# Kernel tuning notes

Hardware: AMD Instinct MI355X
Metric: run time of the kernel (lower is better)

## Reference

```python
import jax, jax.numpy as jnp
import numpy as np

D_MODEL = 768
N_HEADS = 12
D_K = D_MODEL // N_HEADS
NEG = -1e9


def setup_inputs() -> dict:
    key = jax.random.key(0)
    ks = jax.random.split(key, 10)
    B, S = 2, 2048
    x = jax.random.normal(ks[0], (B, S, D_MODEL), dtype=jnp.float32)
    # causal mask, broadcastable over batch and heads
    mask = jnp.tril(jnp.ones((S, S), dtype=jnp.int32))[None, None]
    scale = 1.0 / np.sqrt(D_MODEL)
    def lin(k):
        return jax.random.normal(k, (D_MODEL, D_MODEL), dtype=jnp.float32) * scale
    return {
        "x": x, "mask": mask,
        "wq": lin(ks[1]), "bq": jnp.zeros((D_MODEL,), jnp.float32),
        "wk": lin(ks[2]), "bk": jnp.zeros((D_MODEL,), jnp.float32),
        "wv": lin(ks[3]), "bv": jnp.zeros((D_MODEL,), jnp.float32),
        "wo": lin(ks[4]), "bo": jnp.zeros((D_MODEL,), jnp.float32),
    }


def reference(x, mask, wq, bq, wk, bk, wv, bv, wo, bo):
    B, S, _ = x.shape
    def split_heads(t):  # [B,S,D] -> [B,H,S,dk]
        return t.reshape(B, S, N_HEADS, D_K).transpose(0, 2, 1, 3)
    q = split_heads(x @ wq + bq)
    k = split_heads(x @ wk + bk)
    v = split_heads(x @ wv + bv)
    scores = jnp.einsum("bhqd,bhkd->bhqk", q, k) / jnp.sqrt(jnp.float32(D_K))
    scores = jnp.where(mask == 0, NEG, scores)
    attn = jax.nn.softmax(scores, axis=-1)
    # dropout is identity in eval mode
    ctx = jnp.einsum("bhqk,bhkd->bhqd", attn, v)
    ctx = ctx.transpose(0, 2, 1, 3).reshape(B, S, D_MODEL)
    return ctx @ wo + bo
```

## Files before the change

kernel.cpp:

```cpp
#include <hip/hip_runtime.h>
#include <hip/hip_bf16.h>
#include <stdint.h>

#define DM   768
#define NH   12
#define DKH  64
#define BB   2
#define SS   2048
#define MT   (BB*SS)
#define NQKV (3*DM)

typedef __attribute__((ext_vector_type(8))) short short8;
typedef __attribute__((ext_vector_type(4))) float f32x4;

__device__ __forceinline__ unsigned short f2bf(float f) {
    union { float f; unsigned u; } v; v.f = f;
    unsigned r = v.u + 0x7fffu + ((v.u >> 16) & 1u);
    return (unsigned short)(r >> 16);
}

__device__ __forceinline__ void gload_lds16(const unsigned short* g, unsigned short* l) {
    __builtin_amdgcn_global_load_lds((const __attribute__((address_space(1))) void*)g,
                                     (__attribute__((address_space(3))) void*)l, 16, 0, 0);
}

__launch_bounds__(256)
__global__ void k_conv(const float* __restrict__ x, unsigned short* __restrict__ xb,
                       const float* __restrict__ wq, const float* __restrict__ wk,
                       const float* __restrict__ wv, const float* __restrict__ wo,
                       unsigned short* __restrict__ wT) {
    __shared__ float tile[32][33];
    const int t = threadIdx.x;
    if (blockIdx.x < 3072) {
        int i = blockIdx.x * 256 + t;
        const float4 v = ((const float4*)x)[i];
        ushort4 o;
        o.x = f2bf(v.x); o.y = f2bf(v.y); o.z = f2bf(v.z); o.w = f2bf(v.w);
        ((ushort4*)xb)[i] = o;
    } else {
        const int cid = blockIdx.x - 3072;
        const int sel = cid / 576;
        const int rem = cid - sel * 576;
        const int kb = rem / 24, nb = rem - (rem / 24) * 24;
        const float* w = (sel == 0) ? wq : (sel == 1) ? wk : (sel == 2) ? wv : wo;
        const int k0 = kb * 32, n0 = nb * 32;
        const int tx = t & 31, ty = t >> 5;
        #pragma unroll
        for (int j = 0; j < 4; j++)
            tile[ty + 8*j][tx] = w[(size_t)(k0 + ty + 8*j) * DM + n0 + tx];
        __syncthreads();
        #pragma unroll
        for (int j = 0; j < 4; j++)
            wT[(size_t)(sel*DM + n0 + ty + 8*j) * DM + k0 + tx] = f2bf(tile[tx][ty + 8*j]);
    }
}

__launch_bounds__(256, 4)
__global__ void k_gemm_qkv(const unsigned short* __restrict__ xb,
                           const unsigned short* __restrict__ wT,
                           const float* __restrict__ bq, const float* __restrict__ bk,
                           const float* __restrict__ bv,
                           unsigned short* __restrict__ Qb,
                           unsigned short* __restrict__ Kb,
                           unsigned short* __restrict__ Vt) {
    __shared__ __align__(16) unsigned short As[128*64];
    __shared__ __align__(16) unsigned short Bs[64*64];
    const int t = threadIdx.x;
    const int m0 = blockIdx.x * 128;
    const int n0 = blockIdx.y * 64;
    const int wid = t >> 6, lane = t & 63, q4 = lane >> 4, l16 = lane & 15;
    const int wm = (wid >> 1) * 64, wn = (wid & 1) * 32;

    const int srow = lane >> 3;
    const int scol = ((lane & 7) ^ srow) * 8;
    const unsigned short* Ag = xb + (size_t)(m0 + wid*8 + srow) * DM + scol;
    const unsigned short* Bg = wT + (size_t)(n0 + wid*8 + srow) * DM + scol;
    unsigned short* ldsA = &As[(wid*8)*64];
    unsigned short* ldsB = &Bs[(wid*8)*64];
    const int swz = (l16 & 7) * 8;

    f32x4 acc[4][2];
    for (int i = 0; i < 4; i++) for (int j = 0; j < 2; j++)
        acc[i][j] = (f32x4){0.f, 0.f, 0.f, 0.f};

    for (int kt = 0; kt < DM; kt += 64) {
        #pragma unroll
        for (int j = 0; j < 4; j++)
            gload_lds16(Ag + (size_t)(j*32) * DM + kt, ldsA + j*32*64);
        #pragma unroll
        for (int j = 0; j < 2; j++)
            gload_lds16(Bg + (size_t)(j*32) * DM + kt, ldsB + j*32*64);
        __syncthreads();
        #pragma unroll
        for (int kc = 0; kc < 2; kc++) {
            short8 af[4], bf[2];
            #pragma unroll
            for (int i = 0; i < 4; i++)
                af[i] = *(const short8*)&As[(wm + i*16 + l16)*64 + ((kc*32 + q4*8) ^ swz)];
            #pragma unroll
            for (int i = 0; i < 2; i++)
                bf[i] = *(const short8*)&Bs[(wn + i*16 + l16)*64 + ((kc*32 + q4*8) ^ swz)];
            #pragma unroll
            for (int mi = 0; mi < 4; mi++)
                #pragma unroll
                for (int ni = 0; ni < 2; ni++)
                    acc[mi][ni] = __builtin_amdgcn_mfma_f32_16x16x32_bf16(af[mi], bf[ni], acc[mi][ni], 0, 0, 0);
        }
        __syncthreads();
    }

    const int sel = n0 / DM;
    if (sel < 2) {
        const float* bias = (sel == 0) ? bq : bk;
        for (int ni = 0; ni < 2; ni++) {
            const int col = n0 + wn + ni*16 + l16;
            const int c = col - sel * DM;
            const float bsv = bias[c];
            const int h = c >> 6, d = c & 63;
            for (int mi = 0; mi < 4; mi++) {
                for (int r = 0; r < 4; r++) {
                    const int row = m0 + wm + mi*16 + q4*4 + r;
                    const int b = row >> 11, s = row & 2047;
                    const int bh = b * NH + h;
                    float v = acc[mi][ni][r] + bsv;
                    if (sel == 0) Qb[(bh*SS + s)*DKH + d] = f2bf(v * 0.125f);
                    else          Kb[(bh*SS + s)*DKH + d] = f2bf(v);
                }
            }
        }
    } else {
        const int h  = (n0 - 2*DM) >> 6;
        const int bb = m0 >> 11, sbase = m0 & 2047;
        const int bh = bb * NH + h;
        #pragma unroll
        for (int ni = 0; ni < 2; ni++) {
            const int c = wn + ni*16 + l16;
            const float bsv = bv[h*64 + c];
            #pragma unroll
            for (int mi = 0; mi < 4; mi++) {
                const int rowb = wm + mi*16 + q4*4;
                ushort4 o;
                o.x = f2bf(acc[mi][ni][0] + bsv);
                o.y = f2bf(acc[mi][ni][1] + bsv);
                o.z = f2bf(acc[mi][ni][2] + bsv);
                o.w = f2bf(acc[mi][ni][3] + bsv);
                *(ushort4*)&As[c*128 + (rowb ^ ((c & 7) * 8))] = o;
            }
        }
        __syncthreads();
        const int d = t >> 2, sq = (t & 3) * 32;
        unsigned short* Vg = Vt + ((size_t)bh*DKH + d)*SS + sbase + sq;
        #pragma unroll
        for (int j = 0; j < 4; j++) {
            short8 v = *(const short8*)&As[d*128 + ((sq + j*8) ^ ((d & 7) * 8))];
            *(short8*)&Vg[j*8] = v;
        }
    }
}

__device__ const int UNITS[48] = {
  (15<<16)|(0<<8)|16, (31<<16)|(0<<8)|16, (31<<16)|(16<<8)|32, (30<<16)|(0<<8)|16,
  (14<<16)|(0<<8)|15, (29<<16)|(0<<8)|15, (29<<16)|(15<<8)|30, (28<<16)|(0<<8)|15, (30<<16)|(16<<8)|31,
  (13<<16)|(0<<8)|14, (27<<16)|(0<<8)|14, (27<<16)|(14<<8)|28, (26<<16)|(0<<8)|14, (28<<16)|(15<<8)|29,
  (12<<16)|(0<<8)|13, (25<<16)|(0<<8)|13, (25<<16)|(13<<8)|26, (24<<16)|(0<<8)|13, (26<<16)|(14<<8)|27,
  (11<<16)|(0<<8)|12, (23<<16)|(0<<8)|12, (23<<16)|(12<<8)|24, (22<<16)|(0<<8)|12, (24<<16)|(13<<8)|25,
  (10<<16)|(0<<8)|11, (21<<16)|(0<<8)|11, (21<<16)|(11<<8)|22, (20<<16)|(0<<8)|11, (22<<16)|(12<<8)|23,
  ( 9<<16)|(0<<8)|10, (19<<16)|(0<<8)|10, (19<<16)|(10<<8)|20, (18<<16)|(0<<8)|10, (20<<16)|(11<<8)|21,
  ( 8<<16)|(0<<8)| 9, (17<<16)|(0<<8)| 9, (17<<16)|( 9<<8)|18, (16<<16)|(0<<8)| 9, (18<<16)|(10<<8)|19,
  ( 7<<16)|(0<<8)| 8, (16<<16)|( 9<<8)|17,
  ( 6<<16)|(0<<8)| 7, ( 5<<16)|(0<<8)| 6, ( 4<<16)|(0<<8)| 5, ( 3<<16)|(0<<8)| 4,
  ( 2<<16)|(0<<8)| 3, ( 1<<16)|(0<<8)| 2, ( 0<<16)|(0<<8)| 1,
};

__launch_bounds__(256, 4)
__global__ void k_attn(const unsigned short* __restrict__ Qb,
                       const unsigned short* __restrict__ Kb,
                       const unsigned short* __restrict__ Vt,
                       unsigned short* __restrict__ ctx,
                       float* __restrict__ Opart, float* __restrict__ lpart) {
    __shared__ __align__(16) unsigned short Ks[2][64*64];
    __shared__ __align__(16) unsigned short Vs[2][64*64];
    const int t = threadIdx.x;
    const int wid = t >> 6, lane = t & 63, q4 = lane >> 4, l16 = lane & 15;

    const int lin = blockIdx.x;
    const int bh = lin % 24;
    const int info = UNITS[lin / 24];
    const int qblk = info >> 16, t0 = (info >> 8) & 0xff, t1 = info & 0xff;
    const int b = bh / NH, h = bh - b * NH;
    const int qw = qblk * 64 + wid * 16;

    const unsigned short* Qp = Qb + (size_t)bh * SS * DKH;
    const unsigned short* Kp = Kb + (size_t)bh * SS * DKH;
    const unsigned short* Vp = Vt + (size_t)bh * DKH * SS;

    const int grow = lane >> 3;
    const int gcol = ((lane & 7) ^ grow) * 8;
    const int swz  = (l16 & 7) * 8;

    short8 qf[2];
    qf[0] = *(const short8*)(Qp + (size_t)(qw + l16)*DKH +      q4*8);
    qf[1] = *(const short8*)(Qp + (size_t)(qw + l16)*DKH + 32 + q4*8);

    f32x4 accO[4];
    #pragma unroll
    for (int j = 0; j < 4; j++) accO[j] = (f32x4){0.f, 0.f, 0.f, 0.f};
    float lacc = 0.f;

    {
        const int kb0 = t0 * 64;
        #pragma unroll
        for (int jj = 0; jj < 2; jj++) {
            const int r0 = wid*16 + jj*8;
            gload_lds16(Kp + (size_t)(kb0 + r0 + grow)*DKH + gcol, &Ks[0][r0*64]);
            gload_lds16(Vp + (size_t)(r0 + grow)*SS + kb0 + gcol,  &Vs[0][r0*64]);
        }
    }
    asm volatile("s_waitcnt vmcnt(0)" ::: "memory");
    __syncthreads();

    for (int kt = t0; kt < t1; kt++) {
        const int cb = (kt - t0) & 1, nb = cb ^ 1;
        const bool hasN = (kt + 1 < t1);
        if (hasN) {
            const int kn = (kt + 1) * 64;
            #pragma unroll
            for (int jj = 0; jj < 2; jj++) {
                const int r0 = wid*16 + jj*8;
                gload_lds16(Kp + (size_t)(kn + r0 + grow)*DKH + gcol, &Ks[nb][r0*64]);
                gload_lds16(Vp + (size_t)(r0 + grow)*SS + kn + gcol,  &Vs[nb][r0*64]);
            }
        }
        f32x4 St[4];
        #pragma unroll
        for (int ni = 0; ni < 4; ni++) St[ni] = (f32x4){0.f, 0.f, 0.f, 0.f};
        __builtin_amdgcn_s_setprio(1);
        #pragma unroll
        for (int ni = 0; ni < 4; ni++) {
            const int rbase = (ni*16 + l16) * 64;
            short8 kf0 = *(const short8*)&Ks[cb][rbase + ((     q4*8) ^ swz)];
            short8 kf1 = *(const short8*)&Ks[cb][rbase + ((32 + q4*8) ^ swz)];
            St[ni] = __builtin_amdgcn_mfma_f32_16x16x32_bf16(kf0, qf[0], St[ni], 0, 0, 0);
            St[ni] = __builtin_amdgcn_mfma_f32_16x16x32_bf16(kf1, qf[1], St[ni], 0, 0, 0);
        }
        __builtin_amdgcn_s_setprio(0);
        float p[4][4];
        if (kt < qblk) {
            #pragma unroll
            for (int ni = 0; ni < 4; ni++) {
                #pragma unroll
                for (int r = 0; r < 4; r++) { p[ni][r] = __expf(St[ni][r]); lacc += p[ni][r]; }
            }
        } else {
            const int qrow = qw + l16;
            #pragma unroll
            for (int ni = 0; ni < 4; ni++) {
                const int key0 = kt*64 + ni*16 + q4*4;
                #pragma unroll
                for (int r = 0; r < 4; r++) {
                    p[ni][r] = (key0 + r > qrow) ? 0.f : __expf(St[ni][r]);
                    lacc += p[ni][r];
                }
            }
        }
        union { short8 v; unsigned u[4]; } pf0, pf1;
        {
            union { __hip_bfloat162 v; unsigned u; } w;
            w.v = __float22bfloat162_rn(make_float2(p[0][0], p[0][1])); pf0.u[0] = w.u;
            w.v = __float22bfloat162_rn(make_float2(p[0][2], p[0][3])); pf0.u[1] = w.u;
            w.v = __float22bfloat162_rn(make_float2(p[1][0], p[1][1])); pf0.u[2] = w.u;
            w.v = __float22bfloat162_rn(make_float2(p[1][2], p[1][3])); pf0.u[3] = w.u;
            w.v = __float22bfloat162_rn(make_float2(p[2][0], p[2][1])); pf1.u[0] = w.u;
            w.v = __float22bfloat162_rn(make_float2(p[2][2], p[2][3])); pf1.u[1] = w.u;
            w.v = __float22bfloat162_rn(make_float2(p[3][0], p[3][1])); pf1.u[2] = w.u;
            w.v = __float22bfloat162_rn(make_float2(p[3][2], p[3][3])); pf1.u[3] = w.u;
        }
        __builtin_amdgcn_s_setprio(1);
        #pragma unroll
        for (int ndi = 0; ndi < 4; ndi++) {
            const int rbase = (ndi*16 + l16) * 64;
            union { short8 v; unsigned long long d[2]; } vf0, vf1;
            vf0.d[0] = *(const unsigned long long*)&Vs[cb][rbase + ((     q4*4) ^ swz)];
            vf0.d[1] = *(const unsigned long long*)&Vs[cb][rbase + ((16 + q4*4) ^ swz)];
            vf1.d[0] = *(const unsigned long long*)&Vs[cb][rbase + ((32 + q4*4) ^ swz)];
            vf1.d[1] = *(const unsigned long long*)&Vs[cb][rbase + ((48 + q4*4) ^ swz)];
            accO[ndi] = __builtin_amdgcn_mfma_f32_16x16x32_bf16(vf0.v, pf0.v, accO[ndi], 0, 0, 0);
            accO[ndi] = __builtin_amdgcn_mfma_f32_16x16x32_bf16(vf1.v, pf1.v, accO[ndi], 0, 0, 0);
        }
        __builtin_amdgcn_s_setprio(0);
        asm volatile("s_waitcnt vmcnt(0)" ::: "memory");
        __syncthreads();
    }

    float l = lacc;
    l += __shfl_xor(l, 16);
    l += __shfl_xor(l, 32);

    if (qblk < 16) {
        const float inv = 1.0f / l;
        const size_t row = (size_t)(b*SS + qw + l16);
        #pragma unroll
        for (int ndi = 0; ndi < 4; ndi++) {
            ushort4 o;
            o.x = f2bf(accO[ndi][0] * inv);
            o.y = f2bf(accO[ndi][1] * inv);
            o.z = f2bf(accO[ndi][2] * inv);
            o.w = f2bf(accO[ndi][3] * inv);
            *(ushort4*)&ctx[row*DM + h*64 + ndi*16 + q4*4] = o;
        }
    } else {
        const int pair  = bh * 16 + (qblk - 16);
        const int chunk = (t0 != 0);
        const int qloc  = wid * 16 + l16;
        float* Op = Opart + ((size_t)pair * 2 + chunk) * 4096;
        #pragma unroll
        for (int ndi = 0; ndi < 4; ndi++)
            *(f32x4*)&Op[qloc*64 + ndi*16 + q4*4] = accO[ndi];
        if (q4 == 0) lpart[pair*128 + chunk*64 + qloc] = l;
    }
}

__launch_bounds__(256)
__global__ void k_combine(const float* __restrict__ Opart,
                          const float* __restrict__ lpart,
                          unsigned short* __restrict__ ctx) {
    const int pair = blockIdx.x;
    const int bh = pair >> 4, qblk = 16 + (pair & 15);
    const int b = bh / NH, h = bh - b * NH;
    const int t = threadIdx.x;
    const int q = t >> 2, dg = (t & 3) * 16;
    const float* P0 = Opart + (size_t)pair * 2 * 4096;
    const float* P1 = P0 + 4096;
    const float* L0 = lpart + pair * 128;
    const float inv = 1.0f / (L0[q] + L0[64 + q]);
    const size_t row = (size_t)(b*SS + qblk*64 + q);
    #pragma unroll
    for (int i = 0; i < 4; i++) {
        f32x4 a = *(const f32x4*)&P0[q*64 + dg + i*4];
        f32x4 c = *(const f32x4*)&P1[q*64 + dg + i*4];
        ushort4 o;
        o.x = f2bf((a[0] + c[0]) * inv);
        o.y = f2bf((a[1] + c[1]) * inv);
        o.z = f2bf((a[2] + c[2]) * inv);
        o.w = f2bf((a[3] + c[3]) * inv);
        *(ushort4*)&ctx[row*DM + h*64 + dg + i*4] = o;
    }
}

__launch_bounds__(256, 4)
__global__ void k_gemm_proj(const unsigned short* __restrict__ ctx,
                            const unsigned short* __restrict__ woT,
                            const float* __restrict__ bo,
                            float* __restrict__ out) {
    __shared__ __align__(16) unsigned short As[64*64];
    __shared__ __align__(16) unsigned short Bs[64*64];
    const int t = threadIdx.x;
    const int m0 = blockIdx.x * 64;
    const int n0 = blockIdx.y * 64;
    const int wid = t >> 6, lane = t & 63, q4 = lane >> 4, l16 = lane & 15;
    const int wm = (wid >> 1) * 32, wn = (wid & 1) * 32;

    const int srow = lane >> 3;
    const int scol = ((lane & 7) ^ srow) * 8;
    const unsigned short* Ag = ctx + (size_t)(m0 + wid*8 + srow) * DM + scol;
    const unsigned short* Bg = woT + (size_t)(n0 + wid*8 + srow) * DM + scol;
    unsigned short* ldsA = &As[(wid*8)*64];
    unsigned short* ldsB = &Bs[(wid*8)*64];
    const int swz = (l16 & 7) * 8;

    f32x4 acc[2][2];
    for (int i = 0; i < 2; i++) for (int j = 0; j < 2; j++)
        acc[i][j] = (f32x4){0.f, 0.f, 0.f, 0.f};

    for (int kt = 0; kt < DM; kt += 64) {
        #pragma unroll
        for (int j = 0; j < 2; j++) {
            gload_lds16(Ag + (size_t)(j*32) * DM + kt, ldsA + j*32*64);
            gload_lds16(Bg + (size_t)(j*32) * DM + kt, ldsB + j*32*64);
        }
        __syncthreads();
        #pragma unroll
        for (int kc = 0; kc < 2; kc++) {
            short8 af[2], bf[2];
            #pragma unroll
            for (int i = 0; i < 2; i++)
                af[i] = *(const short8*)&As[(wm + i*16 + l16)*64 + ((kc*32 + q4*8) ^ swz)];
            #pragma unroll
            for (int i = 0; i < 2; i++)
                bf[i] = *(const short8*)&Bs[(wn + i*16 + l16)*64 + ((kc*32 + q4*8) ^ swz)];
            #pragma unroll
            for (int mi = 0; mi < 2; mi++)
                #pragma unroll
                for (int ni = 0; ni < 2; ni++)
                    acc[mi][ni] = __builtin_amdgcn_mfma_f32_16x16x32_bf16(af[mi], bf[ni], acc[mi][ni], 0, 0, 0);
        }
        __syncthreads();
    }

    for (int ni = 0; ni < 2; ni++) {
        const int col = n0 + wn + ni*16 + l16;
        const float bsv = bo[col];
        for (int mi = 0; mi < 2; mi++) {
            for (int r = 0; r < 4; r++) {
                const int row = m0 + wm + mi*16 + q4*4 + r;
                out[(size_t)row * DM + col] = acc[mi][ni][r] + bsv;
            }
        }
    }
}

extern "C" void kernel_launch(void* const* d_in, const int* in_sizes, int n_in,
                              void* d_out, int out_size, void* d_ws, size_t ws_size,
                              hipStream_t stream) {
    const float* x  = (const float*)d_in[0];
    const float* wq = (const float*)d_in[2];
    const float* bq = (const float*)d_in[3];
    const float* wk = (const float*)d_in[4];
    const float* bk = (const float*)d_in[5];
    const float* wv = (const float*)d_in[6];
    const float* bv = (const float*)d_in[7];
    const float* wo = (const float*)d_in[8];
    const float* bo = (const float*)d_in[9];
    float* out = (float*)d_out;

    unsigned short* xb  = (unsigned short*)d_ws;
    unsigned short* wT  = xb + (size_t)MT * DM;
    unsigned short* Qb  = wT + (size_t)4 * DM * DM;
    unsigned short* Kb  = Qb + (size_t)BB * NH * SS * DKH;
    unsigned short* Vt  = Kb + (size_t)BB * NH * SS * DKH;
    unsigned short* ctx = Vt + (size_t)BB * NH * SS * DKH;
    float* Opart = (float*)(ctx + (size_t)MT * DM);
    float* lpart = Opart + (size_t)768 * 4096;

    k_conv<<<3072 + 2304, 256, 0, stream>>>(x, xb, wq, wk, wv, wo, wT);
    dim3 g1(MT / 128, NQKV / 64);
    k_gemm_qkv<<<g1, 256, 0, stream>>>(xb, wT, bq, bk, bv, Qb, Kb, Vt);
    k_attn<<<dim3(1152), 256, 0, stream>>>(Qb, Kb, Vt, ctx, Opart, lpart);
    k_combine<<<dim3(384), 256, 0, stream>>>(Opart, lpart, ctx);
    dim3 g3(MT / 64, DM / 64);
    k_gemm_proj<<<g3, 256, 0, stream>>>(ctx, wT + (size_t)3 * DM * DM, bo, out);
}
```

Before: 158.5 us.

## Use 128-row query blocks with multi-chunk KV split and generalized combine

Each attention block now covers 128 query rows, with every wave handling two 16-row sub-tiles, so each K/V tile loaded into LDS feeds twice as many MFMAs. Long causal rows are split into up to four KV chunks using a new work-unit table, and the combine kernel sums a variable number of partial results. This roughly halves K/V global and LDS traffic per query and rebalances the work across fewer blocks. In exchange it raises register pressure (launch bounds lowered to 3 blocks per unit), lets waves whose rows are already fully masked skip tiles, and makes the partial-result buffer larger.

```diff
diff --git a/kernel.cpp b/kernel.cpp
--- a/kernel.cpp
+++ b/kernel.cpp
@@ -158,21 +158,31 @@
     }
 }
 
-__device__ const int UNITS[48] = {
-  (15<<16)|(0<<8)|16, (31<<16)|(0<<8)|16, (31<<16)|(16<<8)|32, (30<<16)|(0<<8)|16,
-  (14<<16)|(0<<8)|15, (29<<16)|(0<<8)|15, (29<<16)|(15<<8)|30, (28<<16)|(0<<8)|15, (30<<16)|(16<<8)|31,
-  (13<<16)|(0<<8)|14, (27<<16)|(0<<8)|14, (27<<16)|(14<<8)|28, (26<<16)|(0<<8)|14, (28<<16)|(15<<8)|29,
-  (12<<16)|(0<<8)|13, (25<<16)|(0<<8)|13, (25<<16)|(13<<8)|26, (24<<16)|(0<<8)|13, (26<<16)|(14<<8)|27,
-  (11<<16)|(0<<8)|12, (23<<16)|(0<<8)|12, (23<<16)|(12<<8)|24, (22<<16)|(0<<8)|12, (24<<16)|(13<<8)|25,
-  (10<<16)|(0<<8)|11, (21<<16)|(0<<8)|11, (21<<16)|(11<<8)|22, (20<<16)|(0<<8)|11, (22<<16)|(12<<8)|23,
-  ( 9<<16)|(0<<8)|10, (19<<16)|(0<<8)|10, (19<<16)|(10<<8)|20, (18<<16)|(0<<8)|10, (20<<16)|(11<<8)|21,
-  ( 8<<16)|(0<<8)| 9, (17<<16)|(0<<8)| 9, (17<<16)|( 9<<8)|18, (16<<16)|(0<<8)| 9, (18<<16)|(10<<8)|19,
-  ( 7<<16)|(0<<8)| 8, (16<<16)|( 9<<8)|17,
-  ( 6<<16)|(0<<8)| 7, ( 5<<16)|(0<<8)| 6, ( 4<<16)|(0<<8)| 5, ( 3<<16)|(0<<8)| 4,
-  ( 2<<16)|(0<<8)| 3, ( 1<<16)|(0<<8)| 2, ( 0<<16)|(0<<8)| 1,
+#define U(q,c,a,b2) (((q)<<16)|((c)<<12)|((a)<<6)|(b2))
+__device__ const int UNITS[40] = {
+  U(15,0,0,8),  U(15,1,8,16),  U(15,2,16,24), U(15,3,24,32),
+  U(14,0,0,8),  U(14,1,8,16),
+  U(11,0,0,8),  U(11,1,8,16),  U(11,2,16,24),
+  U(10,0,0,8),
+  U(7,0,0,8),   U(7,1,8,16),
+  U(3,0,0,8),
+  U(14,2,16,23), U(14,3,23,30),
+  U(13,0,0,7),  U(13,1,7,14),  U(13,2,14,21), U(13,3,21,28),
+  U(12,0,0,7),  U(12,1,7,14),
+  U(10,1,8,15), U(10,2,15,22),
+  U(9,0,0,7),   U(9,1,7,14),
+  U(6,0,0,7),   U(6,1,7,14),
+  U(12,2,14,20), U(12,3,20,26),
+  U(9,2,14,20),
+  U(8,0,0,6),   U(8,1,6,12),   U(8,2,12,18),
+  U(5,0,0,6),   U(5,1,6,12),
+  U(2,0,0,6),
+  U(4,0,0,5),   U(4,1,5,10),
+  U(1,0,0,4),
+  U(0,0,0,2),
 };
 
-__launch_bounds__(256, 4)
+__launch_bounds__(256, 3)
 __global__ void k_attn(const unsigned short* __restrict__ Qb,
                        const unsigned short* __restrict__ Kb,
                        const unsigned short* __restrict__ Vt,
@@ -186,9 +196,12 @@
     const int lin = blockIdx.x;
     const int bh = lin % 24;
     const int info = UNITS[lin / 24];
-    const int qblk = info >> 16, t0 = (info >> 8) & 0xff, t1 = info & 0xff;
+    const int qsb = info >> 16, ci = (info >> 12) & 0xf;
+    const int t0 = (info >> 6) & 0x3f, t1 = info & 0x3f;
+    const int nch = (2*qsb + 9) >> 3;
     const int b = bh / NH, h = bh - b * NH;
-    const int qw = qblk * 64 + wid * 16;
+    const int qw = qsb*128 + wid*32;
+    const int ktw = (qw + 31) >> 6;
 
     const unsigned short* Qp = Qb + (size_t)bh * SS * DKH;
     const unsigned short* Kp = Kb + (size_t)bh * SS * DKH;
@@ -198,14 +211,19 @@
     const int gcol = ((lane & 7) ^ grow) * 8;
     const int swz  = (l16 & 7) * 8;
 
-    short8 qf[2];
-    qf[0] = *(const short8*)(Qp + (size_t)(qw + l16)*DKH +      q4*8);
-    qf[1] = *(const short8*)(Qp + (size_t)(qw + l16)*DKH + 32 + q4*8);
-
-    f32x4 accO[4];
+    short8 qf[2][2];
     #pragma unroll
-    for (int j = 0; j < 4; j++) accO[j] = (f32x4){0.f, 0.f, 0.f, 0.f};
-    float lacc = 0.f;
+    for (int c = 0; c < 2; c++)
+        #pragma unroll
+        for (int kc = 0; kc < 2; kc++)
+            qf[c][kc] = *(const short8*)(Qp + (size_t)(qw + c*16 + l16)*DKH + kc*32 + q4*8);
+
+    f32x4 accO[2][4];
+    #pragma unroll
+    for (int c = 0; c < 2; c++)
+        #pragma unroll
+        for (int j = 0; j < 4; j++) accO[c][j] = (f32x4){0.f, 0.f, 0.f, 0.f};
+    float lacc[2] = {0.f, 0.f};
 
     {
         const int kb0 = t0 * 64;
@@ -231,92 +249,115 @@
                 gload_lds16(Vp + (size_t)(r0 + grow)*SS + kn + gcol,  &Vs[nb][r0*64]);
             }
         }
-        f32x4 St[4];
-        #pragma unroll
-        for (int ni = 0; ni < 4; ni++) St[ni] = (f32x4){0.f, 0.f, 0.f, 0.f};
-        __builtin_amdgcn_s_setprio(1);
-        #pragma unroll
-        for (int ni = 0; ni < 4; ni++) {
-            const int rbase = (ni*16 + l16) * 64;
-            short8 kf0 = *(const short8*)&Ks[cb][rbase + ((     q4*8) ^ swz)];
-            short8 kf1 = *(const short8*)&Ks[cb][rbase + ((32 + q4*8) ^ swz)];
-            St[ni] = __builtin_amdgcn_mfma_f32_16x16x32_bf16(kf0, qf[0], St[ni], 0, 0, 0);
-            St[ni] = __builtin_amdgcn_mfma_f32_16x16x32_bf16(kf1, qf[1], St[ni], 0, 0, 0);
-        }
-        __builtin_amdgcn_s_setprio(0);
-        float p[4][4];
-        if (kt < qblk) {
+        if (kt <= ktw) {
+            f32x4 St[2][4];
+            #pragma unroll
+            for (int c = 0; c < 2; c++)
+                #pragma unroll
+                for (int ni = 0; ni < 4; ni++) St[c][ni] = (f32x4){0.f, 0.f, 0.f, 0.f};
+            __builtin_amdgcn_s_setprio(1);
             #pragma unroll
             for (int ni = 0; ni < 4; ni++) {
+                const int rbase = (ni*16 + l16) * 64;
+                short8 kf0 = *(const short8*)&Ks[cb][rbase + ((     q4*8) ^ swz)];
+                short8 kf1 = *(const short8*)&Ks[cb][rbase + ((32 + q4*8) ^ swz)];
+                St[0][ni] = __builtin_amdgcn_mfma_f32_16x16x32_bf16(kf0, qf[0][0], St[0][ni], 0, 0, 0);
+                St[0][ni] = __builtin_amdgcn_mfma_f32_16x16x32_bf16(kf1, qf[0][1], St[0][ni], 0, 0, 0);
+                St[1][ni] = __builtin_amdgcn_mfma_f32_16x16x32_bf16(kf0, qf[1][0], St[1][ni], 0, 0, 0);
+                St[1][ni] = __builtin_amdgcn_mfma_f32_16x16x32_bf16(kf1, qf[1][1], St[1][ni], 0, 0, 0);
+            }
+            __builtin_amdgcn_s_setprio(0);
+            float p[2][4][4];
+            if (kt < ktw) {
                 #pragma unroll
-                for (int r = 0; r < 4; r++) { p[ni][r] = __expf(St[ni][r]); lacc += p[ni][r]; }
-            }
-        } else {
-            const int qrow = qw + l16;
-            #pragma unroll
-            for (int ni = 0; ni < 4; ni++) {
-                const int key0 = kt*64 + ni*16 + q4*4;
+                for (int c = 0; c < 2; c++)
+                    #pragma unroll
+                    for (int ni = 0; ni < 4; ni++)
+                        #pragma unroll
+                        for (int r = 0; r < 4; r++) {
+                            p[c][ni][r] = __expf(St[c][ni][r]);
+                            lacc[c] += p[c][ni][r];
+                        }
+            } else {
                 #pragma unroll
-                for (int r = 0; r < 4; r++) {
-                    p[ni][r] = (key0 + r > qrow) ? 0.f : __expf(St[ni][r]);
-                    lacc += p[ni][r];
+                for (int c = 0; c < 2; c++) {
+                    const int qrow = qw + c*16 + l16;
+                    #pragma unroll
+                    for (int ni = 0; ni < 4; ni++) {
+                        const int key0 = kt*64 + ni*16 + q4*4;
+                        #pragma unroll
+                        for (int r = 0; r < 4; r++) {
+                            p[c][ni][r] = (key0 + r > qrow) ? 0.f : __expf(St[c][ni][r]);
+                            lacc[c] += p[c][ni][r];
+                        }
+                    }
                 }
             }
-        }
-        union { short8 v; unsigned u[4]; } pf0, pf1;
-        {
-            union { __hip_bfloat162 v; unsigned u; } w;
-            w.v = __float22bfloat162_rn(make_float2(p[0][0], p[0][1])); pf0.u[0] = w.u;
-            w.v = __float22bfloat162_rn(make_float2(p[0][2], p[0][3])); pf0.u[1] = w.u;
-            w.v = __float22bfloat162_rn(make_float2(p[1][0], p[1][1])); pf0.u[2] = w.u;
-            w.v = __float22bfloat162_rn(make_float2(p[1][2], p[1][3])); pf0.u[3] = w.u;
-            w.v = __float22bfloat162_rn(make_float2(p[2][0], p[2][1])); pf1.u[0] = w.u;
-            w.v = __float22bfloat162_rn(make_float2(p[2][2], p[2][3])); pf1.u[1] = w.u;
-            w.v = __float22bfloat162_rn(make_float2(p[3][0], p[3][1])); pf1.u[2] = w.u;
-            w.v = __float22bfloat162_rn(make_float2(p[3][2], p[3][3])); pf1.u[3] = w.u;
-        }
-        __builtin_amdgcn_s_setprio(1);
-        #pragma unroll
-        for (int ndi = 0; ndi < 4; ndi++) {
-            const int rbase = (ndi*16 + l16) * 64;
-            union { short8 v; unsigned long long d[2]; } vf0, vf1;
-            vf0.d[0] = *(const unsigned long long*)&Vs[cb][rbase + ((     q4*4) ^ swz)];
-            vf0.d[1] = *(const unsigned long long*)&Vs[cb][rbase + ((16 + q4*4) ^ swz)];
-            vf1.d[0] = *(const unsigned long long*)&Vs[cb][rbase + ((32 + q4*4) ^ swz)];
-            vf1.d[1] = *(const unsigned long long*)&Vs[cb][rbase + ((48 + q4*4) ^ swz)];
-            accO[ndi] = __builtin_amdgcn_mfma_f32_16x16x32_bf16(vf0.v, pf0.v, accO[ndi], 0, 0, 0);
-            accO[ndi] = __builtin_amdgcn_mfma_f32_16x16x32_bf16(vf1.v, pf1.v, accO[ndi], 0, 0, 0);
-        }
-        __builtin_amdgcn_s_setprio(0);
+            union { short8 v; unsigned u[4]; } pf[2][2];
+            #pragma unroll
+            for (int c = 0; c < 2; c++) {
+                union { __hip_bfloat162 v; unsigned u; } w;
+                w.v = __float22bfloat162_rn(make_float2(p[c][0][0], p[c][0][1])); pf[c][0].u[0] = w.u;
+                w.v = __float22bfloat162_rn(make_float2(p[c][0][2], p[c][0][3])); pf[c][0].u[1] = w.u;
+                w.v = __float22bfloat162_rn(make_float2(p[c][1][0], p[c][1][1])); pf[c][0].u[2] = w.u;
+                w.v = __float22bfloat162_rn(make_float2(p[c][1][2], p[c][1][3])); pf[c][0].u[3] = w.u;
+                w.v = __float22bfloat162_rn(make_float2(p[c][2][0], p[c][2][1])); pf[c][1].u[0] = w.u;
+                w.v = __float22bfloat162_rn(make_float2(p[c][2][2], p[c][2][3])); pf[c][1].u[1] = w.u;
+                w.v = __float22bfloat162_rn(make_float2(p[c][3][0], p[c][3][1])); pf[c][1].u[2] = w.u;
+                w.v = __float22bfloat162_rn(make_float2(p[c][3][2], p[c][3][3])); pf[c][1].u[3] = w.u;
+            }
+            __builtin_amdgcn_s_setprio(1);
+            #pragma unroll
+            for (int ndi = 0; ndi < 4; ndi++) {
+                const int rbase = (ndi*16 + l16) * 64;
+                union { short8 v; unsigned long long d[2]; } vf0, vf1;
+                vf0.d[0] = *(const unsigned long long*)&Vs[cb][rbase + ((     q4*4) ^ swz)];
+                vf0.d[1] = *(const unsigned long long*)&Vs[cb][rbase + ((16 + q4*4) ^ swz)];
+                vf1.d[0] = *(const unsigned long long*)&Vs[cb][rbase + ((32 + q4*4) ^ swz)];
+                vf1.d[1] = *(const unsigned long long*)&Vs[cb][rbase + ((48 + q4*4) ^ swz)];
+                accO[0][ndi] = __builtin_amdgcn_mfma_f32_16x16x32_bf16(vf0.v, pf[0][0].v, accO[0][ndi], 0, 0, 0);
+                accO[0][ndi] = __builtin_amdgcn_mfma_f32_16x16x32_bf16(vf1.v, pf[0][1].v, accO[0][ndi], 0, 0, 0);
+                accO[1][ndi] = __builtin_amdgcn_mfma_f32_16x16x32_bf16(vf0.v, pf[1][0].v, accO[1][ndi], 0, 0, 0);
+                accO[1][ndi] = __builtin_amdgcn_mfma_f32_16x16x32_bf16(vf1.v, pf[1][1].v, accO[1][ndi], 0, 0, 0);
+            }
+            __builtin_amdgcn_s_setprio(0);
+        }
         asm volatile("s_waitcnt vmcnt(0)" ::: "memory");
         __syncthreads();
     }
 
-    float l = lacc;
-    l += __shfl_xor(l, 16);
-    l += __shfl_xor(l, 32);
-
-    if (qblk < 16) {
-        const float inv = 1.0f / l;
-        const size_t row = (size_t)(b*SS + qw + l16);
-        #pragma unroll
-        for (int ndi = 0; ndi < 4; ndi++) {
-            ushort4 o;
-            o.x = f2bf(accO[ndi][0] * inv);
-            o.y = f2bf(accO[ndi][1] * inv);
-            o.z = f2bf(accO[ndi][2] * inv);
-            o.w = f2bf(accO[ndi][3] * inv);
-            *(ushort4*)&ctx[row*DM + h*64 + ndi*16 + q4*4] = o;
+    if (nch == 1) {
+        #pragma unroll
+        for (int c = 0; c < 2; c++) {
+            float l = lacc[c];
+            l += __shfl_xor(l, 16);
+            l += __shfl_xor(l, 32);
+            const float inv = 1.0f / l;
+            const size_t row = (size_t)(b*SS + qw + c*16 + l16);
+            #pragma unroll
+            for (int ndi = 0; ndi < 4; ndi++) {
+                ushort4 o;
+                o.x = f2bf(accO[c][ndi][0] * inv);
+                o.y = f2bf(accO[c][ndi][1] * inv);
+                o.z = f2bf(accO[c][ndi][2] * inv);
+                o.w = f2bf(accO[c][ndi][3] * inv);
+                *(ushort4*)&ctx[row*DM + h*64 + ndi*16 + q4*4] = o;
+            }
         }
     } else {
-        const int pair  = bh * 16 + (qblk - 16);
-        const int chunk = (t0 != 0);
-        const int qloc  = wid * 16 + l16;
-        float* Op = Opart + ((size_t)pair * 2 + chunk) * 4096;
-        #pragma unroll
-        for (int ndi = 0; ndi < 4; ndi++)
-            *(f32x4*)&Op[qloc*64 + ndi*16 + q4*4] = accO[ndi];
-        if (q4 == 0) lpart[pair*128 + chunk*64 + qloc] = l;
+        const int slot = (bh*16 + qsb)*4 + ci;
+        float* Op = Opart + (size_t)slot * 8192;
+        #pragma unroll
+        for (int c = 0; c < 2; c++) {
+            float l = lacc[c];
+            l += __shfl_xor(l, 16);
+            l += __shfl_xor(l, 32);
+            const int qloc = wid*32 + c*16 + l16;
+            #pragma unroll
+            for (int ndi = 0; ndi < 4; ndi++)
+                *(f32x4*)&Op[qloc*64 + ndi*16 + q4*4] = accO[c][ndi];
+            if (q4 == 0) lpart[slot*128 + qloc] = l;
+        }
     }
 }
 
@@ -325,25 +366,33 @@
                           const float* __restrict__ lpart,
                           unsigned short* __restrict__ ctx) {
     const int pair = blockIdx.x;
-    const int bh = pair >> 4, qblk = 16 + (pair & 15);
+    const int bh = pair / 12, qsb = 4 + pair % 12;
+    const int nch = (2*qsb + 9) >> 3;
     const int b = bh / NH, h = bh - b * NH;
+    const int s0 = (bh*16 + qsb)*4;
     const int t = threadIdx.x;
-    const int q = t >> 2, dg = (t & 3) * 16;
-    const float* P0 = Opart + (size_t)pair * 2 * 4096;
-    const float* P1 = P0 + 4096;
-    const float* L0 = lpart + pair * 128;
-    const float inv = 1.0f / (L0[q] + L0[64 + q]);
-    const size_t row = (size_t)(b*SS + qblk*64 + q);
     #pragma unroll
-    for (int i = 0; i < 4; i++) {
-        f32x4 a = *(const f32x4*)&P0[q*64 + dg + i*4];
-        f32x4 c = *(const f32x4*)&P1[q*64 + dg + i*4];
-        ushort4 o;
-        o.x = f2bf((a[0] + c[0]) * inv);
-        o.y = f2bf((a[1] + c[1]) * inv);
-        o.z = f2bf((a[2] + c[2]) * inv);
-        o.w = f2bf((a[3] + c[3]) * inv);
-        *(ushort4*)&ctx[row*DM + h*64 + dg + i*4] = o;
+    for (int it = 0; it < 2; it++) {
+        const int q = (t >> 2) + it*64;
+        const int dg = (t & 3) * 16;
+        float lsum = 0.f;
+        for (int ci = 0; ci < nch; ci++) lsum += lpart[(s0 + ci)*128 + q];
+        const float inv = 1.0f / lsum;
+        const size_t row = (size_t)(b*SS + qsb*128 + q);
+        #pragma unroll
+        for (int i = 0; i < 4; i++) {
+            f32x4 a = (f32x4){0.f, 0.f, 0.f, 0.f};
+            for (int ci = 0; ci < nch; ci++) {
+                f32x4 c = *(const f32x4*)&Opart[(size_t)(s0 + ci)*8192 + q*64 + dg + i*4];
+                a[0] += c[0]; a[1] += c[1]; a[2] += c[2]; a[3] += c[3];
+            }
+            ushort4 o;
+            o.x = f2bf(a[0] * inv);
+            o.y = f2bf(a[1] * inv);
+            o.z = f2bf(a[2] * inv);
+            o.w = f2bf(a[3] * inv);
+            *(ushort4*)&ctx[row*DM + h*64 + dg + i*4] = o;
+        }
     }
 }
 
@@ -430,13 +479,13 @@
     unsigned short* Vt  = Kb + (size_t)BB * NH * SS * DKH;
     unsigned short* ctx = Vt + (size_t)BB * NH * SS * DKH;
     float* Opart = (float*)(ctx + (size_t)MT * DM);
-    float* lpart = Opart + (size_t)768 * 4096;
+    float* lpart = Opart + (size_t)24 * 16 * 4 * 8192;
 
     k_conv<<<3072 + 2304, 256, 0, stream>>>(x, xb, wq, wk, wv, wo, wT);
     dim3 g1(MT / 128, NQKV / 64);
     k_gemm_qkv<<<g1, 256, 0, stream>>>(xb, wT, bq, bk, bv, Qb, Kb, Vt);
-    k_attn<<<dim3(1152), 256, 0, stream>>>(Qb, Kb, Vt, ctx, Opart, lpart);
-    k_combine<<<dim3(384), 256, 0, stream>>>(Opart, lpart, ctx);
+    k_attn<<<dim3(960), 256, 0, stream>>>(Qb, Kb, Vt, ctx, Opart, lpart);
+    k_combine<<<dim3(288), 256, 0, stream>>>(Opart, lpart, ctx);
     dim3 g3(MT / 64, DM / 64);
     k_gemm_proj<<<g3, 256, 0, stream>>>(ctx, wT + (size_t)3 * DM * DM, bo, out);
 }
```

After: 169.7 us. 1.07x slower.
